# Kernel tuning notes

Hardware: AMD Instinct MI355X
Metric: run time of the kernel (lower is better)

## Reference

```python
import jax, jax.numpy as jnp
import numpy as np

H = W = 224
N_LM = 8
BLOCK = 3  # patch is [x-3:x+3, y-3:y+3] -> 6x6


def _clip_coords(lm_float):
    # lm_float: [B, 16] normalized landmarks in [0,1]
    c = (lm_float * 224.0).astype(jnp.int32)
    c = jnp.where(c >= 219, 200, c)
    c = jnp.where(c <= 5, 8, c)
    return c.reshape(c.shape[0], N_LM, 2)


def _gather_patches(pred_map, coords):
    # pred_map: [B,1,H,W], coords: [B,8,2] int32 -> [B,8,36]
    B = pred_map.shape[0]
    x = coords[..., 0]  # [B,8]
    y = coords[..., 1]
    offs = jnp.arange(-BLOCK, BLOCK)  # 6 offsets
    xs = x[..., None] + offs          # [B,8,6]
    ys = y[..., None] + offs          # [B,8,6]
    b = jnp.arange(B)[:, None, None, None]
    # vectorized gather replacing the per-sample/per-landmark python loop
    patches = pred_map[b, 0, xs[:, :, :, None], ys[:, :, None, :]]  # [B,8,6,6]
    return patches.reshape(B, N_LM, (2 * BLOCK) ** 2)


def setup_inputs() -> dict:
    key = jax.random.key(0)
    ks = jax.random.split(key, 8)
    B = 512
    pred_map = jax.random.normal(ks[0], (B, 1, H, W), dtype=jnp.float32)
    Landmarks_GT = jax.random.uniform(ks[1], (B, 16), dtype=jnp.float32)
    d_in = H * W  # 50176
    s1 = 1.0 / np.sqrt(d_in)
    s2 = 1.0 / np.sqrt(512)
    s3 = 1.0 / np.sqrt(256)
    W1 = jax.random.uniform(ks[2], (d_in, 512), jnp.float32, -s1, s1)
    b1 = jax.random.uniform(ks[3], (512,), jnp.float32, -s1, s1)
    W2 = jax.random.uniform(ks[4], (512, 256), jnp.float32, -s2, s2)
    b2 = jax.random.uniform(ks[5], (256,), jnp.float32, -s2, s2)
    W3 = jax.random.uniform(ks[6], (256, 16), jnp.float32, -s3, s3)
    b3 = jax.random.uniform(ks[7], (16,), jnp.float32, -s3, s3)
    return {"pred_map": pred_map, "Landmarks_GT": Landmarks_GT,
            "W1": W1, "b1": b1, "W2": W2, "b2": b2, "W3": W3, "b3": b3}


def reference(pred_map, Landmarks_GT, W1, b1, W2, b2, W3, b3):
    B = pred_map.shape[0]
    # GT landmark patch gather
    gt_coords = _clip_coords(Landmarks_GT)
    GT_patch = _gather_patches(pred_map, gt_coords)  # [B,8,36]
    # MLP_Grah_Second on flattened pred_map
    flat = pred_map.reshape(B, -1)                   # [B,50176]
    h = jax.nn.relu(flat @ W1 + b1)
    h = jax.nn.relu(h @ W2 + b2)
    pred = jax.nn.sigmoid(h @ W3 + b3)               # [B,16]
    # predicted landmark patch gather
    pr_coords = _clip_coords(pred)
    Pred_patch = _gather_patches(pred_map, pr_coords)  # [B,8,36]
    return pred, GT_patch, Pred_patch
```

## Files before the change

kernel.cpp:

```cpp
#include <hip/hip_runtime.h>
#include <math.h>

typedef __fp16   h16x2 __attribute__((ext_vector_type(2)));
typedef _Float16 f16x8 __attribute__((ext_vector_type(8)));
typedef __attribute__((ext_vector_type(4))) float f32x4;

#define KDIM 50176
#define NDIM 512
#define MDIM 512
#define BM 256
#define BN 128
#define BK 32

__device__ __forceinline__ void split_pair(float a, float b, unsigned& hw, unsigned& lw) {
    h16x2 hp = __builtin_amdgcn_cvt_pkrtz(a, b);
    float ra = (a - (float)hp[0]) * 2048.0f;
    float rb = (b - (float)hp[1]) * 2048.0f;
    h16x2 lp;
    lp[0] = (__fp16)ra;
    lp[1] = (__fp16)rb;
    union { h16x2 v; unsigned u; } cu;
    cu.v = hp; hw = cu.u;
    cu.v = lp; lw = cu.u;
}

__global__ __launch_bounds__(512, 2) void gemm1_mfma(
    const float* __restrict__ A,
    const float* __restrict__ W,
    float* __restrict__ part,
    int steps)
{
    __shared__ unsigned short Ahs[2][256][40];
    __shared__ unsigned short Als[2][256][40];
    __shared__ unsigned short Bhs[2][128][40];
    __shared__ unsigned short Bls[2][128][40];

    const int t = threadIdx.x;
    const int bm = blockIdx.x, bn = blockIdx.y, z = blockIdx.z;
    const int kbase = z * steps * BK;

    const int lane = t & 63, wave = t >> 6;
    const int wm = wave >> 1, wn = wave & 1;
    const int l15 = lane & 15, lh = lane >> 4;

    const bool isW = (t < 256);
    const int u = isW ? t : (t - 256);
    const int wkb = u & 7, wn0 = (u >> 3) * 4;
    const int achunk = u & 7, arow0 = u >> 3;

    f32x4 acc0[4][4], acc1[4][4];
#pragma unroll
    for (int i = 0; i < 4; ++i)
#pragma unroll
        for (int j = 0; j < 4; ++j) { acc0[i][j] = (f32x4)0.f; acc1[i][j] = (f32x4)0.f; }

    float4 reg[8];
    auto gload = [&](int s) {
        const int k0 = kbase + s * BK;
        if (isW) {
            const float* Wb = W + (size_t)k0 * NDIM + bn * BN + wn0;
#pragma unroll
            for (int i = 0; i < 4; ++i)
                reg[i] = *(const float4*)(Wb + (size_t)(wkb * 4 + i) * NDIM);
        } else {
            const float* Ab = A + (size_t)(bm * BM) * KDIM + k0 + achunk * 4;
#pragma unroll
            for (int j = 0; j < 8; ++j)
                reg[j] = *(const float4*)(Ab + (size_t)(arow0 + 32 * j) * KDIM);
        }
    };

    auto stage = [&](int buf) {
        if (isW) {
#pragma unroll
            for (int j = 0; j < 4; ++j) {
                unsigned h01, l01, h23, l23;
                float v0 = ((const float*)&reg[0])[j] * 64.0f;
                float v1 = ((const float*)&reg[1])[j] * 64.0f;
                float v2 = ((const float*)&reg[2])[j] * 64.0f;
                float v3 = ((const float*)&reg[3])[j] * 64.0f;
                split_pair(v0, v1, h01, l01);
                split_pair(v2, v3, h23, l23);
                *(uint2*)&Bhs[buf][wn0 + j][wkb * 4] = make_uint2(h01, h23);
                *(uint2*)&Bls[buf][wn0 + j][wkb * 4] = make_uint2(l01, l23);
            }
        } else {
#pragma unroll
            for (int j = 0; j < 8; ++j) {
                unsigned h01, l01, h23, l23;
                split_pair(reg[j].x, reg[j].y, h01, l01);
                split_pair(reg[j].z, reg[j].w, h23, l23);
                *(uint2*)&Ahs[buf][arow0 + 32 * j][achunk * 4] = make_uint2(h01, h23);
                *(uint2*)&Als[buf][arow0 + 32 * j][achunk * 4] = make_uint2(l01, l23);
            }
        }
    };

    auto compute = [&](int buf) {
        f16x8 bhf[4], blf[4];
#pragma unroll
        for (int nf = 0; nf < 4; ++nf) {
            bhf[nf] = *(const f16x8*)&Bhs[buf][wn * 64 + nf * 16 + l15][lh * 8];
            blf[nf] = *(const f16x8*)&Bls[buf][wn * 64 + nf * 16 + l15][lh * 8];
        }
#pragma unroll
        for (int mf = 0; mf < 4; ++mf) {
            f16x8 ah = *(const f16x8*)&Ahs[buf][wm * 64 + mf * 16 + l15][lh * 8];
            f16x8 al = *(const f16x8*)&Als[buf][wm * 64 + mf * 16 + l15][lh * 8];
#pragma unroll
            for (int nf = 0; nf < 4; ++nf) {
                acc0[mf][nf] = __builtin_amdgcn_mfma_f32_16x16x32_f16(ah, bhf[nf], acc0[mf][nf], 0, 0, 0);
                acc1[mf][nf] = __builtin_amdgcn_mfma_f32_16x16x32_f16(ah, blf[nf], acc1[mf][nf], 0, 0, 0);
                acc1[mf][nf] = __builtin_amdgcn_mfma_f32_16x16x32_f16(al, bhf[nf], acc1[mf][nf], 0, 0, 0);
            }
        }
    };

    gload(0);
    stage(0);
    __syncthreads();
    int cur = 0;
    for (int s = 0; s < steps; ++s) {
        if (s + 1 < steps) gload(s + 1);
        compute(cur);
        if (s + 1 < steps) stage(cur ^ 1);
        __syncthreads();
        cur ^= 1;
    }

    const float c0 = 1.0f / 64.0f;
    const float c1 = 1.0f / 131072.0f;
    float* Cp = part + (size_t)z * (MDIM * NDIM);
    const int row0 = bm * BM + wm * 64;
    const int col0 = bn * BN + wn * 64;
#pragma unroll
    for (int mf = 0; mf < 4; ++mf)
#pragma unroll
        for (int nf = 0; nf < 4; ++nf) {
            const int r0 = row0 + mf * 16 + lh * 4;
            const int c = col0 + nf * 16 + l15;
#pragma unroll
            for (int r = 0; r < 4; ++r)
                Cp[(size_t)(r0 + r) * NDIM + c] = acc0[mf][nf][r] * c0 + acc1[mf][nf][r] * c1;
        }
}

__global__ __launch_bounds__(256) void reduce_bias_relu(
    const float4* __restrict__ part, const float* __restrict__ b1,
    float4* __restrict__ h1, int S)
{
    int i = blockIdx.x * 256 + threadIdx.x;
    float4 s = make_float4(0.f, 0.f, 0.f, 0.f);
    for (int z = 0; z < S; ++z) {
        float4 v = part[(size_t)z * 65536 + i];
        s.x += v.x; s.y += v.y; s.z += v.z; s.w += v.w;
    }
    int nb = (i & 127) * 4;
    s.x = fmaxf(s.x + b1[nb + 0], 0.f);
    s.y = fmaxf(s.y + b1[nb + 1], 0.f);
    s.z = fmaxf(s.z + b1[nb + 2], 0.f);
    s.w = fmaxf(s.w + b1[nb + 3], 0.f);
    h1[i] = s;
}

__global__ __launch_bounds__(256) void gemm2_k(
    const float* __restrict__ h1, const float* __restrict__ W2,
    const float* __restrict__ b2, float* __restrict__ h2)
{
    int g = blockIdx.x * 256 + threadIdx.x;
    int m = g >> 8, n = g & 255;
    const float* a = h1 + (size_t)m * 512;
    float sum = 0.f;
#pragma unroll 8
    for (int k = 0; k < 512; ++k) sum = fmaf(a[k], W2[(size_t)k * 256 + n], sum);
    sum += b2[n];
    h2[g] = fmaxf(sum, 0.f);
}

__global__ __launch_bounds__(256) void gemm3_sig(
    const float* __restrict__ h2, const float* __restrict__ W3,
    const float* __restrict__ b3, float* __restrict__ pred)
{
    int g = blockIdx.x * 256 + threadIdx.x;
    int m = g >> 4, j = g & 15;
    const float* a = h2 + (size_t)m * 256;
    float sum = 0.f;
#pragma unroll 8
    for (int k = 0; k < 256; ++k) sum = fmaf(a[k], W3[(size_t)k * 16 + j], sum);
    sum += b3[j];
    pred[g] = 1.f / (1.f + expf(-sum));
}

__device__ __forceinline__ int clip_coord(float v) {
    int c = (int)(v * 224.0f);
    if (c >= 219) c = 200;
    if (c <= 5)   c = 8;
    return c;
}

__global__ void patches_k(
    const float* __restrict__ pm, const float* __restrict__ gt,
    const float* __restrict__ pred, float* __restrict__ out)
{
    const int b = blockIdx.x;
    const int t = threadIdx.x;
    const int lm = t / 36, cell = t % 36;
    const int dx = cell / 6 - 3, dy = cell % 6 - 3;
    const float* pmb = pm + (size_t)b * 50176;
    {
        int cx = clip_coord(gt[b * 16 + lm * 2 + 0]);
        int cy = clip_coord(gt[b * 16 + lm * 2 + 1]);
        out[8192 + b * 288 + t] = pmb[(cx + dx) * 224 + (cy + dy)];
    }
    {
        int cx = clip_coord(pred[b * 16 + lm * 2 + 0]);
        int cy = clip_coord(pred[b * 16 + lm * 2 + 1]);
        out[8192 + 147456 + b * 288 + t] = pmb[(cx + dx) * 224 + (cy + dy)];
    }
}

extern "C" void kernel_launch(void* const* d_in, const int* in_sizes, int n_in,
                              void* d_out, int out_size, void* d_ws, size_t ws_size,
                              hipStream_t stream)
{
    const float* pred_map = (const float*)d_in[0];
    const float* gt       = (const float*)d_in[1];
    const float* W1       = (const float*)d_in[2];
    const float* b1       = (const float*)d_in[3];
    const float* W2       = (const float*)d_in[4];
    const float* b2       = (const float*)d_in[5];
    const float* W3       = (const float*)d_in[6];
    const float* b3       = (const float*)d_in[7];
    float* out = (float*)d_out;

    float* h1   = (float*)d_ws;
    float* h2   = h1 + 262144;
    float* part = h2 + 131072;

    static const int cand[] = {32, 16, 8, 4, 2, 1};
    int S = 1;
    for (int i = 0; i < 6; ++i) {
        size_t need = (size_t)(393216 + (size_t)cand[i] * 262144) * sizeof(float);
        if (need <= ws_size) { S = cand[i]; break; }
    }
    const int steps = 1568 / S;

    hipLaunchKernelGGL(gemm1_mfma, dim3(2, 4, S), dim3(512), 0, stream,
                       pred_map, W1, part, steps);
    hipLaunchKernelGGL(reduce_bias_relu, dim3(256), dim3(256), 0, stream,
                       (const float4*)part, b1, (float4*)h1, S);
    hipLaunchKernelGGL(gemm2_k, dim3(131072 / 256), dim3(256), 0, stream, h1, W2, b2, h2);
    hipLaunchKernelGGL(gemm3_sig, dim3(8192 / 256), dim3(256), 0, stream, h2, W3, b3, out);
    hipLaunchKernelGGL(patches_k, dim3(512), dim3(288), 0, stream, pred_map, gt, out, out);
}
```

Before: 165.3 us.

## Shrink GEMM1 tile to 128x128, single-buffer LDS, remap workgroups by XCD

The first GEMM's M tile drops from 256 to 128 rows, and the launch grid becomes a 1-D grid of 16*S workgroups. Block indices are remapped so that consecutive workgroups are spread across the eight XCDs. LDS goes from double to single buffering, with an extra barrier each step, so more workgroups fit per CU (launch bounds 512,4). W loads change from float4 rows to strided scalar loads. The aim is more occupancy and parallelism, at the cost of lower per-tile reuse, twice the A/W traffic per output, and extra synchronization.

```diff
diff --git a/kernel.cpp b/kernel.cpp
--- a/kernel.cpp
+++ b/kernel.cpp
@@ -8,7 +8,7 @@
 #define KDIM 50176
 #define NDIM 512
 #define MDIM 512
-#define BM 256
+#define BM 128
 #define BN 128
 #define BK 32
 
@@ -24,117 +24,124 @@
     cu.v = lp; lw = cu.u;
 }
 
-__global__ __launch_bounds__(512, 2) void gemm1_mfma(
+__global__ __launch_bounds__(512, 4) void gemm1_mfma(
     const float* __restrict__ A,
     const float* __restrict__ W,
     float* __restrict__ part,
-    int steps)
-{
-    __shared__ unsigned short Ahs[2][256][40];
-    __shared__ unsigned short Als[2][256][40];
-    __shared__ unsigned short Bhs[2][128][40];
-    __shared__ unsigned short Bls[2][128][40];
+    int steps, int S)
+{
+    __shared__ unsigned short Ahs[128][40];
+    __shared__ unsigned short Als[128][40];
+    __shared__ unsigned short Bhs[128][40];
+    __shared__ unsigned short Bls[128][40];
 
     const int t = threadIdx.x;
-    const int bm = blockIdx.x, bn = blockIdx.y, z = blockIdx.z;
+
+    const int nwg = 16 * S;
+    int l = blockIdx.x;
+    if ((nwg & 7) == 0) l = (l & 7) * (nwg >> 3) + (l >> 3);
+    const int bm = l & 3, bn = (l >> 2) & 3, z = l >> 4;
+
     const int kbase = z * steps * BK;
+    const int bmBase = bm * BM, bnBase = bn * BN;
 
     const int lane = t & 63, wave = t >> 6;
-    const int wm = wave >> 1, wn = wave & 1;
+    const int wm = wave >> 1, wn2 = wave & 1;
     const int l15 = lane & 15, lh = lane >> 4;
 
     const bool isW = (t < 256);
     const int u = isW ? t : (t - 256);
-    const int wkb = u & 7, wn0 = (u >> 3) * 4;
+    const int wnr = u & 31, wkc = u >> 5;
     const int achunk = u & 7, arow0 = u >> 3;
 
-    f32x4 acc0[4][4], acc1[4][4];
-#pragma unroll
-    for (int i = 0; i < 4; ++i)
+    f32x4 acc0[2][4], acc1[2][4];
+#pragma unroll
+    for (int i = 0; i < 2; ++i)
 #pragma unroll
         for (int j = 0; j < 4; ++j) { acc0[i][j] = (f32x4)0.f; acc1[i][j] = (f32x4)0.f; }
 
-    float4 reg[8];
+    float4 aReg[4];
+    float  wRegv[16];
+
     auto gload = [&](int s) {
         const int k0 = kbase + s * BK;
         if (isW) {
-            const float* Wb = W + (size_t)k0 * NDIM + bn * BN + wn0;
+            const float* Wb = W + (size_t)k0 * NDIM + bnBase + wnr;
 #pragma unroll
             for (int i = 0; i < 4; ++i)
-                reg[i] = *(const float4*)(Wb + (size_t)(wkb * 4 + i) * NDIM);
+#pragma unroll
+                for (int j = 0; j < 4; ++j)
+                    wRegv[i * 4 + j] = Wb[(size_t)(wkc * 4 + i) * NDIM + 32 * j];
         } else {
-            const float* Ab = A + (size_t)(bm * BM) * KDIM + k0 + achunk * 4;
-#pragma unroll
-            for (int j = 0; j < 8; ++j)
-                reg[j] = *(const float4*)(Ab + (size_t)(arow0 + 32 * j) * KDIM);
+            const float* Ab = A + (size_t)(bmBase + arow0) * KDIM + k0 + achunk * 4;
+#pragma unroll
+            for (int j = 0; j < 4; ++j)
+                aReg[j] = *(const float4*)(Ab + (size_t)(32 * j) * KDIM);
         }
     };
 
-    auto stage = [&](int buf) {
+    auto stage = [&]() {
         if (isW) {
 #pragma unroll
             for (int j = 0; j < 4; ++j) {
                 unsigned h01, l01, h23, l23;
-                float v0 = ((const float*)&reg[0])[j] * 64.0f;
-                float v1 = ((const float*)&reg[1])[j] * 64.0f;
-                float v2 = ((const float*)&reg[2])[j] * 64.0f;
-                float v3 = ((const float*)&reg[3])[j] * 64.0f;
-                split_pair(v0, v1, h01, l01);
-                split_pair(v2, v3, h23, l23);
-                *(uint2*)&Bhs[buf][wn0 + j][wkb * 4] = make_uint2(h01, h23);
-                *(uint2*)&Bls[buf][wn0 + j][wkb * 4] = make_uint2(l01, l23);
+                split_pair(wRegv[0 * 4 + j] * 64.0f, wRegv[1 * 4 + j] * 64.0f, h01, l01);
+                split_pair(wRegv[2 * 4 + j] * 64.0f, wRegv[3 * 4 + j] * 64.0f, h23, l23);
+                *(uint2*)&Bhs[wnr + 32 * j][wkc * 4] = make_uint2(h01, h23);
+                *(uint2*)&Bls[wnr + 32 * j][wkc * 4] = make_uint2(l01, l23);
             }
         } else {
 #pragma unroll
-            for (int j = 0; j < 8; ++j) {
+            for (int j = 0; j < 4; ++j) {
                 unsigned h01, l01, h23, l23;
-                split_pair(reg[j].x, reg[j].y, h01, l01);
-                split_pair(reg[j].z, reg[j].w, h23, l23);
-                *(uint2*)&Ahs[buf][arow0 + 32 * j][achunk * 4] = make_uint2(h01, h23);
-                *(uint2*)&Als[buf][arow0 + 32 * j][achunk * 4] = make_uint2(l01, l23);
+                split_pair(aReg[j].x, aReg[j].y, h01, l01);
+                split_pair(aReg[j].z, aReg[j].w, h23, l23);
+                *(uint2*)&Ahs[arow0 + 32 * j][achunk * 4] = make_uint2(h01, h23);
+                *(uint2*)&Als[arow0 + 32 * j][achunk * 4] = make_uint2(l01, l23);
             }
         }
     };
 
-    auto compute = [&](int buf) {
-        f16x8 bhf[4], blf[4];
+    auto compute = [&]() {
+        f16x8 ah[2], al[2];
+#pragma unroll
+        for (int mf = 0; mf < 2; ++mf) {
+            ah[mf] = *(const f16x8*)&Ahs[wm * 32 + mf * 16 + l15][lh * 8];
+            al[mf] = *(const f16x8*)&Als[wm * 32 + mf * 16 + l15][lh * 8];
+        }
 #pragma unroll
         for (int nf = 0; nf < 4; ++nf) {
-            bhf[nf] = *(const f16x8*)&Bhs[buf][wn * 64 + nf * 16 + l15][lh * 8];
-            blf[nf] = *(const f16x8*)&Bls[buf][wn * 64 + nf * 16 + l15][lh * 8];
-        }
-#pragma unroll
-        for (int mf = 0; mf < 4; ++mf) {
-            f16x8 ah = *(const f16x8*)&Ahs[buf][wm * 64 + mf * 16 + l15][lh * 8];
-            f16x8 al = *(const f16x8*)&Als[buf][wm * 64 + mf * 16 + l15][lh * 8];
-#pragma unroll
-            for (int nf = 0; nf < 4; ++nf) {
-                acc0[mf][nf] = __builtin_amdgcn_mfma_f32_16x16x32_f16(ah, bhf[nf], acc0[mf][nf], 0, 0, 0);
-                acc1[mf][nf] = __builtin_amdgcn_mfma_f32_16x16x32_f16(ah, blf[nf], acc1[mf][nf], 0, 0, 0);
-                acc1[mf][nf] = __builtin_amdgcn_mfma_f32_16x16x32_f16(al, bhf[nf], acc1[mf][nf], 0, 0, 0);
+            f16x8 bh = *(const f16x8*)&Bhs[wn2 * 64 + nf * 16 + l15][lh * 8];
+            f16x8 bl = *(const f16x8*)&Bls[wn2 * 64 + nf * 16 + l15][lh * 8];
+#pragma unroll
+            for (int mf = 0; mf < 2; ++mf) {
+                acc0[mf][nf] = __builtin_amdgcn_mfma_f32_16x16x32_f16(ah[mf], bh, acc0[mf][nf], 0, 0, 0);
+                acc1[mf][nf] = __builtin_amdgcn_mfma_f32_16x16x32_f16(ah[mf], bl, acc1[mf][nf], 0, 0, 0);
+                acc1[mf][nf] = __builtin_amdgcn_mfma_f32_16x16x32_f16(al[mf], bh, acc1[mf][nf], 0, 0, 0);
             }
         }
     };
 
     gload(0);
-    stage(0);
+    stage();
     __syncthreads();
-    int cur = 0;
     for (int s = 0; s < steps; ++s) {
         if (s + 1 < steps) gload(s + 1);
-        compute(cur);
-        if (s + 1 < steps) stage(cur ^ 1);
+        compute();
         __syncthreads();
-        cur ^= 1;
+        if (s + 1 < steps) {
+            stage();
+            __syncthreads();
+        }
     }
 
     const float c0 = 1.0f / 64.0f;
     const float c1 = 1.0f / 131072.0f;
     float* Cp = part + (size_t)z * (MDIM * NDIM);
-    const int row0 = bm * BM + wm * 64;
-    const int col0 = bn * BN + wn * 64;
-#pragma unroll
-    for (int mf = 0; mf < 4; ++mf)
+    const int row0 = bmBase + wm * 32;
+    const int col0 = bnBase + wn2 * 64;
+#pragma unroll
+    for (int mf = 0; mf < 2; ++mf)
 #pragma unroll
         for (int nf = 0; nf < 4; ++nf) {
             const int r0 = row0 + mf * 16 + lh * 4;
@@ -245,8 +252,8 @@
     }
     const int steps = 1568 / S;
 
-    hipLaunchKernelGGL(gemm1_mfma, dim3(2, 4, S), dim3(512), 0, stream,
-                       pred_map, W1, part, steps);
+    hipLaunchKernelGGL(gemm1_mfma, dim3(16 * S), dim3(512), 0, stream,
+                       pred_map, W1, part, steps, S);
     hipLaunchKernelGGL(reduce_bias_relu, dim3(256), dim3(256), 0, stream,
                        (const float4*)part, b1, (float4*)h1, S);
     hipLaunchKernelGGL(gemm2_k, dim3(131072 / 256), dim3(256), 0, stream, h1, W2, b2, h2);
```

Measured after the change: 195.2 us. 18.1% more time.

## Interleave next-tile LDS staging with MFMA groups and raise priority during MFMAs

Applied to the files above, without the earlier changes.

The main loop now loads all A fragments up front and walks the N fragments one at a time. After each group of MFMAs it converts and stores part of the prefetched next tile into shared memory, instead of staging the whole tile after all compute. MFMA bursts are wrapped in s_setprio(1)/s_setprio(0) so the scheduler favours matrix issue. The aim is to hide the fp32-to-fp16 split conversion and the LDS writes behind matrix work, at the cost of holding more A fragments in registers at once.

```diff
diff --git a/kernel.cpp b/kernel.cpp
--- a/kernel.cpp
+++ b/kernel.cpp
@@ -40,7 +40,7 @@
     const int kbase = z * steps * BK;
 
     const int lane = t & 63, wave = t >> 6;
-    const int wm = wave >> 1, wn = wave & 1;
+    const int wm = wave >> 1, wn2 = wave & 1;
     const int l15 = lane & 15, lh = lane >> 4;
 
     const bool isW = (t < 256);
@@ -70,60 +70,69 @@
         }
     };
 
-    auto stage = [&](int buf) {
+    auto stageA = [&](int buf, int j) {
+        unsigned h01, l01, h23, l23;
+        split_pair(reg[j].x, reg[j].y, h01, l01);
+        split_pair(reg[j].z, reg[j].w, h23, l23);
+        *(uint2*)&Ahs[buf][arow0 + 32 * j][achunk * 4] = make_uint2(h01, h23);
+        *(uint2*)&Als[buf][arow0 + 32 * j][achunk * 4] = make_uint2(l01, l23);
+    };
+    auto stageW = [&](int buf, int j) {
+        unsigned h01, l01, h23, l23;
+        split_pair(((const float*)&reg[0])[j] * 64.0f, ((const float*)&reg[1])[j] * 64.0f, h01, l01);
+        split_pair(((const float*)&reg[2])[j] * 64.0f, ((const float*)&reg[3])[j] * 64.0f, h23, l23);
+        *(uint2*)&Bhs[buf][wn0 + j][wkb * 4] = make_uint2(h01, h23);
+        *(uint2*)&Bls[buf][wn0 + j][wkb * 4] = make_uint2(l01, l23);
+    };
+    auto full_stage = [&](int buf) {
         if (isW) {
 #pragma unroll
-            for (int j = 0; j < 4; ++j) {
-                unsigned h01, l01, h23, l23;
-                float v0 = ((const float*)&reg[0])[j] * 64.0f;
-                float v1 = ((const float*)&reg[1])[j] * 64.0f;
-                float v2 = ((const float*)&reg[2])[j] * 64.0f;
-                float v3 = ((const float*)&reg[3])[j] * 64.0f;
-                split_pair(v0, v1, h01, l01);
-                split_pair(v2, v3, h23, l23);
-                *(uint2*)&Bhs[buf][wn0 + j][wkb * 4] = make_uint2(h01, h23);
-                *(uint2*)&Bls[buf][wn0 + j][wkb * 4] = make_uint2(l01, l23);
-            }
+            for (int j = 0; j < 4; ++j) stageW(buf, j);
         } else {
 #pragma unroll
-            for (int j = 0; j < 8; ++j) {
-                unsigned h01, l01, h23, l23;
-                split_pair(reg[j].x, reg[j].y, h01, l01);
-                split_pair(reg[j].z, reg[j].w, h23, l23);
-                *(uint2*)&Ahs[buf][arow0 + 32 * j][achunk * 4] = make_uint2(h01, h23);
-                *(uint2*)&Als[buf][arow0 + 32 * j][achunk * 4] = make_uint2(l01, l23);
-            }
-        }
-    };
-
-    auto compute = [&](int buf) {
-        f16x8 bhf[4], blf[4];
-#pragma unroll
-        for (int nf = 0; nf < 4; ++nf) {
-            bhf[nf] = *(const f16x8*)&Bhs[buf][wn * 64 + nf * 16 + l15][lh * 8];
-            blf[nf] = *(const f16x8*)&Bls[buf][wn * 64 + nf * 16 + l15][lh * 8];
-        }
-#pragma unroll
-        for (int mf = 0; mf < 4; ++mf) {
-            f16x8 ah = *(const f16x8*)&Ahs[buf][wm * 64 + mf * 16 + l15][lh * 8];
-            f16x8 al = *(const f16x8*)&Als[buf][wm * 64 + mf * 16 + l15][lh * 8];
-#pragma unroll
-            for (int nf = 0; nf < 4; ++nf) {
-                acc0[mf][nf] = __builtin_amdgcn_mfma_f32_16x16x32_f16(ah, bhf[nf], acc0[mf][nf], 0, 0, 0);
-                acc1[mf][nf] = __builtin_amdgcn_mfma_f32_16x16x32_f16(ah, blf[nf], acc1[mf][nf], 0, 0, 0);
-                acc1[mf][nf] = __builtin_amdgcn_mfma_f32_16x16x32_f16(al, bhf[nf], acc1[mf][nf], 0, 0, 0);
-            }
+            for (int j = 0; j < 8; ++j) stageA(buf, j);
         }
     };
 
     gload(0);
-    stage(0);
+    full_stage(0);
     __syncthreads();
     int cur = 0;
     for (int s = 0; s < steps; ++s) {
-        if (s + 1 < steps) gload(s + 1);
-        compute(cur);
-        if (s + 1 < steps) stage(cur ^ 1);
+        const bool pf = (s + 1 < steps);
+        if (pf) gload(s + 1);
+
+        f16x8 ah[4], al[4];
+#pragma unroll
+        for (int mf = 0; mf < 4; ++mf) {
+            ah[mf] = *(const f16x8*)&Ahs[cur][wm * 64 + mf * 16 + l15][lh * 8];
+            al[mf] = *(const f16x8*)&Als[cur][wm * 64 + mf * 16 + l15][lh * 8];
+        }
+
+#pragma unroll
+        for (int nf = 0; nf < 4; ++nf) {
+            f16x8 bh = *(const f16x8*)&Bhs[cur][wn2 * 64 + nf * 16 + l15][lh * 8];
+            f16x8 bl = *(const f16x8*)&Bls[cur][wn2 * 64 + nf * 16 + l15][lh * 8];
+            __builtin_amdgcn_s_setprio(1);
+#pragma unroll
+            for (int mf = 0; mf < 4; ++mf) {
+                acc0[mf][nf] = __builtin_amdgcn_mfma_f32_16x16x32_f16(ah[mf], bh, acc0[mf][nf], 0, 0, 0);
+                acc1[mf][nf] = __builtin_amdgcn_mfma_f32_16x16x32_f16(ah[mf], bl, acc1[mf][nf], 0, 0, 0);
+                acc1[mf][nf] = __builtin_amdgcn_mfma_f32_16x16x32_f16(al[mf], bh, acc1[mf][nf], 0, 0, 0);
+            }
+            __builtin_amdgcn_s_setprio(0);
+            if (pf) {
+                if (isW) {
+                    if (nf == 0) {
+#pragma unroll
+                        for (int j = 0; j < 4; ++j) stageW(cur ^ 1, j);
+                    }
+                } else {
+                    stageA(cur ^ 1, 2 * nf);
+                    stageA(cur ^ 1, 2 * nf + 1);
+                }
+            }
+        }
         __syncthreads();
         cur ^= 1;
     }
@@ -132,7 +141,7 @@
     const float c1 = 1.0f / 131072.0f;
     float* Cp = part + (size_t)z * (MDIM * NDIM);
     const int row0 = bm * BM + wm * 64;
-    const int col0 = bn * BN + wn * 64;
+    const int col0 = bn * BN + wn2 * 64;
 #pragma unroll
     for (int mf = 0; mf < 4; ++mf)
 #pragma unroll
```

Measured after the change: 215.6 us. 30.4% more time.
